# Optimization experiments

Hardware: AMD Instinct MI355X
Metric: run time of the kernel (lower is better)

## Reference

```python
import jax, jax.numpy as jnp
import numpy as np
import math

D_MODEL = 1024
EXPAND = 2
D_INNER = EXPAND * D_MODEL  # 2048
D_STATE = 16
D_CONV = 4
DT_RANK = math.ceil(D_MODEL / 16)  # 64
BATCH = 1
SEQLEN = 2048


def _silu(x):
    return x * jax.nn.sigmoid(x)


def _selective_scan(u, delta, A, B, C, D, z, delta_bias):
    """u, delta, z: (b,d,l); A: (d,n); B, C: (b,n,l); D, delta_bias: (d)."""
    delta = jax.nn.softplus(delta + delta_bias[None, :, None])        # (b,d,l)
    dA = jnp.exp(jnp.einsum('bdl,dn->lbdn', delta, A))                # (l,b,d,n)
    dBu = jnp.einsum('bdl,bnl->lbdn', delta * u, B)                   # (l,b,d,n)
    Ct = jnp.transpose(C, (2, 0, 1))                                  # (l,b,n)

    def step(h, inp):
        dA_t, dBu_t, C_t = inp
        h = dA_t * h + dBu_t                                          # (b,d,n)
        y = jnp.einsum('bdn,bn->bd', h, C_t)
        return h, y

    h0 = jnp.zeros((u.shape[0], u.shape[1], A.shape[1]), dtype=u.dtype)
    _, ys = jax.lax.scan(step, h0, (dA, dBu, Ct))                     # ys: (l,b,d)
    y = jnp.transpose(ys, (1, 2, 0))                                  # (b,d,l)
    y = y + D[:, None] * u
    return y * _silu(z)


def _causal_conv1d(x, conv_w, conv_b):
    """x: (b,d,l); conv_w: (d,w); conv_b: (d). Depthwise causal conv."""
    x_pad = jnp.pad(x, ((0, 0), (0, 0), (D_CONV - 1, 0)))
    kernel = conv_w[:, None, :]  # (d, 1, w)
    y = jax.lax.conv_general_dilated(
        x_pad, kernel, window_strides=(1,), padding='VALID',
        dimension_numbers=('NCH', 'OIH', 'NCH'),
        feature_group_count=D_INNER)
    return y + conv_b[None, :, None]


def setup_inputs() -> dict:
    key = jax.random.key(0)
    ks = jax.random.split(key, 12)
    hidden_states = jax.random.normal(ks[0], (BATCH, SEQLEN, D_MODEL), dtype=jnp.float32)
    in_proj_w = jax.random.normal(ks[1], (2 * D_INNER, D_MODEL), dtype=jnp.float32) * (D_MODEL ** -0.5)
    conv_w = jax.random.normal(ks[2], (D_INNER, D_CONV), dtype=jnp.float32) * (D_CONV ** -0.5)
    conv_b = jnp.zeros((D_INNER,), dtype=jnp.float32)
    dt_std = DT_RANK ** -0.5

    def dt_bias(k):
        dt = jnp.exp(jax.random.uniform(k, (D_INNER,)) * (math.log(0.1) - math.log(0.001)) + math.log(0.001))
        dt = jnp.clip(dt, 1e-4, None)
        return dt + jnp.log(-jnp.expm1(-dt))  # inverse softplus

    A_log = jnp.log(jnp.broadcast_to(jnp.arange(1, D_STATE + 1, dtype=jnp.float32), (D_INNER, D_STATE)))
    x1_proj_w = jax.random.normal(ks[3], (DT_RANK + 2 * D_STATE, D_INNER), dtype=jnp.float32) * (D_INNER ** -0.5)
    dt1_proj_w = jax.random.uniform(ks[4], (D_INNER, DT_RANK), minval=-dt_std, maxval=dt_std)
    dt1_proj_b = dt_bias(ks[5])
    x2_proj_w = jax.random.normal(ks[6], (DT_RANK + 2 * D_STATE, D_INNER), dtype=jnp.float32) * (D_INNER ** -0.5)
    dt2_proj_w = jax.random.uniform(ks[7], (D_INNER, DT_RANK), minval=-dt_std, maxval=dt_std)
    dt2_proj_b = dt_bias(ks[8])
    out_proj_w = jax.random.normal(ks[9], (D_MODEL, D_INNER), dtype=jnp.float32) * (D_INNER ** -0.5)
    return {
        'hidden_states': hidden_states,
        'in_proj_w': in_proj_w, 'conv_w': conv_w, 'conv_b': conv_b,
        'x1_proj_w': x1_proj_w, 'dt1_proj_w': dt1_proj_w, 'dt1_proj_b': dt1_proj_b,
        'A1_log': A_log, 'D1': jnp.ones((D_INNER,), dtype=jnp.float32),
        'x2_proj_w': x2_proj_w, 'dt2_proj_w': dt2_proj_w, 'dt2_proj_b': dt2_proj_b,
        'A2_log': A_log, 'D2': jnp.ones((D_INNER,), dtype=jnp.float32),
        'out_proj_w': out_proj_w,
    }


def reference(hidden_states, in_proj_w, conv_w, conv_b,
              x1_proj_w, dt1_proj_w, dt1_proj_b, A1_log, D1,
              x2_proj_w, dt2_proj_w, dt2_proj_b, A2_log, D2,
              out_proj_w):
    # in_proj: (b,l,d) @ W^T -> (b, 2*d_inner, l)
    xz = jnp.einsum('bld,ed->bel', hidden_states, in_proj_w)
    x, z = jnp.split(xz, 2, axis=1)                                   # (b,d_inner,l) each
    A1 = -jnp.exp(A1_log.astype(jnp.float32))
    A2 = -jnp.exp(A2_log.astype(jnp.float32))
    x = _silu(_causal_conv1d(x, conv_w, conv_b))                      # (b,d_inner,l)

    def branch_params(xp_w, dtp_w):
        dbl = jnp.einsum('bdl,kd->bkl', x, xp_w)                      # (b, r+2n, l)
        dt, Bm, Cm = jnp.split(dbl, [DT_RANK, DT_RANK + D_STATE], axis=1)
        dt = jnp.einsum('brl,dr->bdl', dt, dtp_w)
        return dt, Bm, Cm

    dt1, B1, C1 = branch_params(x1_proj_w, dt1_proj_w)
    dt2, B2, C2 = branch_params(x2_proj_w, dt2_proj_w)
    y1 = _selective_scan(x, dt1, A1, B1, C1, D1.astype(jnp.float32), z, dt1_proj_b.astype(jnp.float32))
    y2 = _selective_scan(x, dt2, A2, B2, C2, D2.astype(jnp.float32), z, dt2_proj_b.astype(jnp.float32))
    y = y1 - y2                                                       # (b,d_inner,l)
    out = jnp.einsum('bdl,od->blo', y, out_proj_w)                    # (b,l,d_model)
    return out
```

## Files before the change

kernel.cpp:

```cpp
#include <hip/hip_runtime.h>
#include <math.h>

#define SEQ 2048
#define DMODEL 1024
#define DIN 2048
#define NST 16
#define DTR 64
#define CH 32
#define NCH (SEQ / CH)
#define LOG2E 1.4426950408889634f

typedef __attribute__((ext_vector_type(8))) _Float16 f16x8;
typedef __attribute__((ext_vector_type(4))) float f32x4;

__device__ __forceinline__ ushort f2h(float f) {
  union { _Float16 h; ushort u; } c; c.h = (_Float16)f; return c.u;
}
__device__ __forceinline__ float h2f(ushort u) {
  union { ushort u; _Float16 h; } c; c.u = u; return (float)c.h;
}
__device__ __forceinline__ float splus(float v) {
  return v > 20.f ? v : log1pf(__expf(v));
}
__device__ __forceinline__ void powers16(float e, float* p) {
  float e2 = e * e, e4 = e2 * e2, e8 = e4 * e4;
  p[0] = e;       p[1] = e2;       p[2] = e2 * e;   p[3] = e4;
  p[4] = e4 * e;  p[5] = e4 * e2;  p[6] = e4 * p[2]; p[7] = e8;
  p[8] = e8 * e;  p[9] = e8 * e2;  p[10] = e8 * p[2]; p[11] = e8 * e4;
  p[12] = e8 * p[4]; p[13] = e8 * p[5]; p[14] = e8 * p[6]; p[15] = e8 * e8;
}

#define GLL(g, l) __builtin_amdgcn_global_load_lds( \
    (const __attribute__((address_space(1))) void*)(g), \
    (__attribute__((address_space(3))) void*)(l), 16, 0, 0)

template<int BM, int BN, int SPLITK, int MODE>
__global__ __launch_bounds__(256, 2) void gemm3p(const ushort* __restrict__ Ahi,
                                                 const ushort* __restrict__ Alo,
                                                 const ushort* __restrict__ Bhi,
                                                 const ushort* __restrict__ Blo,
                                                 float* __restrict__ C,
                                                 int M, int N, int K) {
  constexpr int BK = 32;
  constexpr int WM = BM / 2, WN = BN / 2, TM = WM / 16, TN = WN / 16;
  constexpr int SA = BM / 16, SB = BN / 16;
  constexpr bool dropB = (MODE == 2);
  __shared__ __align__(16) ushort sAh[BM * BK], sAl[BM * BK];
  __shared__ __align__(16) ushort sBh[BN * BK];
  __shared__ __align__(16) ushort sBl[dropB ? 16 : BN * BK];
  const int tid = threadIdx.x, wid = tid >> 6, lane = tid & 63;
  const int m0 = blockIdx.y * BM, n0 = blockIdx.x * BN;
  const int Kc = K / SPLITK, kbeg = blockIdx.z * Kc;
  const int wm0 = (wid >> 1) * WM, wn0 = (wid & 1) * WN;
  const int fr = lane & 15;
  const int lrow = lane >> 2;
  const int lkc = (lane & 3) ^ ((lane >> 3) & 3);
  const int fpo = fr * 32 + (((lane >> 4) ^ ((lane >> 1) & 3)) * 8);

  f32x4 acc[TM][TN], accL[TM][TN];
#pragma unroll
  for (int mi = 0; mi < TM; ++mi)
#pragma unroll
    for (int ni = 0; ni < TN; ++ni)
#pragma unroll
      for (int r = 0; r < 4; ++r) { acc[mi][ni][r] = 0.f; accL[mi][ni][r] = 0.f; }

  for (int k0 = 0; k0 < Kc; k0 += BK) {
    __syncthreads();
    const int kg = kbeg + k0 + lkc * 8;
#pragma unroll
    for (int i = 0; i < SA / 4; ++i) {
      const int seg = wid * (SA / 4) + i;
      const size_t ga = (size_t)(m0 + seg * 16 + lrow) * K + kg;
      GLL(&Ahi[ga], &sAh[seg * 512]);
      GLL(&Alo[ga], &sAl[seg * 512]);
    }
#pragma unroll
    for (int i = 0; i < SB / 4; ++i) {
      const int seg = wid * (SB / 4) + i;
      const size_t ga = (size_t)(n0 + seg * 16 + lrow) * K + kg;
      GLL(&Bhi[ga], &sBh[seg * 512]);
      if constexpr (!dropB) GLL(&Blo[ga], &sBl[seg * 512]);
    }
    __syncthreads();

    f16x8 ah[TM], al[TM], bh[TN], bl[TN];
#pragma unroll
    for (int mi = 0; mi < TM; ++mi) {
      const int r = (wm0 / 16 + mi) * 512 + fpo;
      ah[mi] = *(const f16x8*)&sAh[r];
      al[mi] = *(const f16x8*)&sAl[r];
    }
#pragma unroll
    for (int ni = 0; ni < TN; ++ni) {
      const int r = (wn0 / 16 + ni) * 512 + fpo;
      bh[ni] = *(const f16x8*)&sBh[r];
      if constexpr (!dropB) bl[ni] = *(const f16x8*)&sBl[r];
    }
#pragma unroll
    for (int mi = 0; mi < TM; ++mi)
#pragma unroll
      for (int ni = 0; ni < TN; ++ni) {
        acc[mi][ni] = __builtin_amdgcn_mfma_f32_16x16x32_f16(ah[mi], bh[ni], acc[mi][ni], 0, 0, 0);
        accL[mi][ni] = __builtin_amdgcn_mfma_f32_16x16x32_f16(al[mi], bh[ni], accL[mi][ni], 0, 0, 0);
        if constexpr (!dropB)
          accL[mi][ni] = __builtin_amdgcn_mfma_f32_16x16x32_f16(ah[mi], bl[ni], accL[mi][ni], 0, 0, 0);
      }
  }

  float* __restrict__ Co = C + (size_t)blockIdx.z * M * N;
#pragma unroll
  for (int mi = 0; mi < TM; ++mi)
#pragma unroll
    for (int ni = 0; ni < TN; ++ni)
#pragma unroll
      for (int r = 0; r < 4; ++r)
        Co[(size_t)(m0 + wm0 + mi * 16 + (lane >> 4) * 4 + r) * N + n0 + wn0 + ni * 16 + fr] =
            acc[mi][ni][r] + accL[mi][ni][r] * (1.f / 2048.f);
}

__global__ __launch_bounds__(256, 2) void dt_mfma(const ushort* __restrict__ dtT_hi,
                                                  const ushort* __restrict__ dtT_lo,
                                                  const ushort* __restrict__ dw_hi,
                                                  const ushort* __restrict__ dw_lo,
                                                  const float* __restrict__ b1,
                                                  const float* __restrict__ b2,
                                                  float* __restrict__ o1,
                                                  float* __restrict__ o2) {
  const int br = blockIdx.z;
  const ushort* __restrict__ Ah = dtT_hi + (size_t)br * 131072;
  const ushort* __restrict__ Al_ = dtT_lo + (size_t)br * 131072;
  const ushort* __restrict__ Bh = dw_hi + (size_t)br * 131072;
  const ushort* __restrict__ Bl = dw_lo + (size_t)br * 131072;
  const float* __restrict__ bias = br ? b2 : b1;
  float* __restrict__ o = br ? o2 : o1;
  __shared__ __align__(16) ushort sAh[128 * 32], sAl[128 * 32];
  __shared__ __align__(16) ushort sBh[128 * 32], sBl[128 * 32];
  const int tid = threadIdx.x, wid = tid >> 6, lane = tid & 63;
  const int m0 = blockIdx.y * 128, n0 = blockIdx.x * 128;
  const int wm0 = (wid >> 1) * 64, wn0 = (wid & 1) * 64;
  const int fr = lane & 15;
  const int lrow = lane >> 2;
  const int lkc = (lane & 3) ^ ((lane >> 3) & 3);
  const int fpo = fr * 32 + (((lane >> 4) ^ ((lane >> 1) & 3)) * 8);

  f32x4 acc[4][4], accL[4][4];
#pragma unroll
  for (int mi = 0; mi < 4; ++mi)
#pragma unroll
    for (int ni = 0; ni < 4; ++ni)
#pragma unroll
      for (int r = 0; r < 4; ++r) { acc[mi][ni][r] = 0.f; accL[mi][ni][r] = 0.f; }

  for (int k0 = 0; k0 < 64; k0 += 32) {
    __syncthreads();
    const int kg = k0 + lkc * 8;
#pragma unroll
    for (int i = 0; i < 2; ++i) {
      const int seg = wid * 2 + i;
      const size_t ga = (size_t)(m0 + seg * 16 + lrow) * 64 + kg;
      GLL(&Ah[ga], &sAh[seg * 512]);
      GLL(&Al_[ga], &sAl[seg * 512]);
      const size_t gb = (size_t)(n0 + seg * 16 + lrow) * 64 + kg;
      GLL(&Bh[gb], &sBh[seg * 512]);
      GLL(&Bl[gb], &sBl[seg * 512]);
    }
    __syncthreads();

    f16x8 ah[4], al[4], bh[4], bl[4];
#pragma unroll
    for (int mi = 0; mi < 4; ++mi) {
      const int r = (wm0 / 16 + mi) * 512 + fpo;
      ah[mi] = *(const f16x8*)&sAh[r];
      al[mi] = *(const f16x8*)&sAl[r];
    }
#pragma unroll
    for (int ni = 0; ni < 4; ++ni) {
      const int r = (wn0 / 16 + ni) * 512 + fpo;
      bh[ni] = *(const f16x8*)&sBh[r];
      bl[ni] = *(const f16x8*)&sBl[r];
    }
#pragma unroll
    for (int mi = 0; mi < 4; ++mi)
#pragma unroll
      for (int ni = 0; ni < 4; ++ni) {
        acc[mi][ni] = __builtin_amdgcn_mfma_f32_16x16x32_f16(ah[mi], bh[ni], acc[mi][ni], 0, 0, 0);
        accL[mi][ni] = __builtin_amdgcn_mfma_f32_16x16x32_f16(al[mi], bh[ni], accL[mi][ni], 0, 0, 0);
        accL[mi][ni] = __builtin_amdgcn_mfma_f32_16x16x32_f16(ah[mi], bl[ni], accL[mi][ni], 0, 0, 0);
      }
  }

#pragma unroll
  for (int ni = 0; ni < 4; ++ni) {
    const int n = n0 + wn0 + ni * 16 + fr;
    const float bv = bias[n];
#pragma unroll
    for (int mi = 0; mi < 4; ++mi)
#pragma unroll
      for (int r = 0; r < 4; ++r) {
        const int m = m0 + wm0 + mi * 16 + (lane >> 4) * 4 + r;
        o[(size_t)m * DIN + n] = splus(acc[mi][ni][r] + accL[mi][ni][r] * (1.f / 2048.f) + bv);
      }
  }
}

__device__ __forceinline__ void split_store4h(float4 v, ushort* hi, ushort* lo, size_t i) {
  ushort h0 = f2h(v.x), h1 = f2h(v.y), h2 = f2h(v.z), h3 = f2h(v.w);
  *(ushort4*)&hi[i] = make_ushort4(h0, h1, h2, h3);
  *(ushort4*)&lo[i] = make_ushort4(f2h((v.x - h2f(h0)) * 2048.f), f2h((v.y - h2f(h1)) * 2048.f),
                                   f2h((v.z - h2f(h2)) * 2048.f), f2h((v.w - h2f(h3)) * 2048.f));
}

__global__ __launch_bounds__(256) void cvt_fused(const float* __restrict__ inw,
                                                 const float* __restrict__ hid,
                                                 const float* __restrict__ x1w,
                                                 const float* __restrict__ x2w,
                                                 const float* __restrict__ dtw1,
                                                 const float* __restrict__ dtw2,
                                                 ushort* __restrict__ w_hi, ushort* __restrict__ w_lo,
                                                 ushort* __restrict__ h_hi,
                                                 ushort* __restrict__ wx_hi, ushort* __restrict__ wx_lo,
                                                 ushort* __restrict__ dw_hi, ushort* __restrict__ dw_lo) {
  const int q = blockIdx.x * 256 + threadIdx.x;
  if (q >= 1048576 && q < 1572864) {
    const size_t i = (size_t)(q - 1048576) * 4;
    float4 v = *(const float4*)&hid[i];
    *(ushort4*)&h_hi[i] = make_ushort4(f2h(v.x), f2h(v.y), f2h(v.z), f2h(v.w));
    return;
  }
  const float* src; ushort* dhi; ushort* dlo; int base;
  if (q < 1048576)       { src = inw; dhi = w_hi;  dlo = w_lo;  base = q; }
  else if (q < 1622016)  { src = x1w; dhi = wx_hi; dlo = wx_lo; base = q - 1572864; }
  else if (q < 1671168)  { src = x2w; dhi = wx_hi + 196608; dlo = wx_lo + 196608; base = q - 1622016; }
  else if (q < 1703936)  { src = dtw1; dhi = dw_hi; dlo = dw_lo; base = q - 1671168; }
  else                   { src = dtw2; dhi = dw_hi + 131072; dlo = dw_lo + 131072; base = q - 1703936; }
  const size_t i = (size_t)base * 4;
  split_store4h(*(const float4*)&src[i], dhi, dlo, i);
}

__global__ __launch_bounds__(256) void reduce_out(const float* __restrict__ p,
                                                  float* __restrict__ o, int n) {
  const int i = (blockIdx.x * 256 + threadIdx.x) * 4;
  if (i >= n) return;
  float4 a = *(const float4*)&p[i];
  float4 b = *(const float4*)&p[(size_t)n + i];
  float4 c = *(const float4*)&p[(size_t)2 * n + i];
  float4 d = *(const float4*)&p[(size_t)3 * n + i];
  *(float4*)&o[i] = make_float4(a.x + b.x + c.x + d.x, a.y + b.y + c.y + d.y,
                                a.z + b.z + c.z + d.z, a.w + b.w + c.w + d.w);
}

__global__ __launch_bounds__(256) void conv_tr_kernel(const float* __restrict__ xz,
                                                      const float* __restrict__ cw,
                                                      const float* __restrict__ cb,
                                                      ushort* __restrict__ xcT_hi,
                                                      ushort* __restrict__ xcT_lo,
                                                      float* __restrict__ zsT) {
  const int l0 = blockIdx.x * 64, d0 = blockIdx.y * 64;
  const int tid = threadIdx.x;
  __shared__ float xin[64][68];
  __shared__ float To[64][65];
  __shared__ float cwS[64][4];
  __shared__ float cbS[64];

  for (int i = tid; i < 1024; i += 256) {
    const int d = i >> 4, q = i & 15;
    float4 v = *(const float4*)&xz[(size_t)(d0 + d) * SEQ + l0 + q * 4];
    xin[d][3 + q * 4 + 0] = v.x; xin[d][3 + q * 4 + 1] = v.y;
    xin[d][3 + q * 4 + 2] = v.z; xin[d][3 + q * 4 + 3] = v.w;
  }
  if (tid < 192) {
    const int j = tid >> 6, d = tid & 63;
    const int l = l0 - 3 + j;
    xin[d][j] = (l >= 0) ? xz[(size_t)(d0 + d) * SEQ + l] : 0.f;
  }
  if (tid < 64) {
    cbS[tid] = cb[d0 + tid];
    float4 w = *(const float4*)&cw[(d0 + tid) * 4];
    cwS[tid][0] = w.x; cwS[tid][1] = w.y; cwS[tid][2] = w.z; cwS[tid][3] = w.w;
  }
  __syncthreads();

  for (int i = tid; i < 4096; i += 256) {
    const int d = i >> 6, l = i & 63;
    float a = cbS[d] + cwS[d][0] * xin[d][l] + cwS[d][1] * xin[d][l + 1] +
              cwS[d][2] * xin[d][l + 2] + cwS[d][3] * xin[d][l + 3];
    To[d][l] = a / (1.f + __expf(-a));
  }
  __syncthreads();

  for (int i = tid; i < 4096; i += 256) {
    const int l = i >> 6, dd = i & 63;
    float v = To[dd][l];
    ushort h = f2h(v);
    xcT_hi[(size_t)(l0 + l) * DIN + d0 + dd] = h;
    xcT_lo[(size_t)(l0 + l) * DIN + d0 + dd] = f2h((v - h2f(h)) * 2048.f);
  }
  __syncthreads();

  for (int i = tid; i < 1024; i += 256) {
    const int d = i >> 4, q = i & 15;
    float4 v = *(const float4*)&xz[(size_t)(DIN + d0 + d) * SEQ + l0 + q * 4];
    To[d][q * 4 + 0] = v.x / (1.f + __expf(-v.x));
    To[d][q * 4 + 1] = v.y / (1.f + __expf(-v.y));
    To[d][q * 4 + 2] = v.z / (1.f + __expf(-v.z));
    To[d][q * 4 + 3] = v.w / (1.f + __expf(-v.w));
  }
  __syncthreads();
  for (int i = tid; i < 4096; i += 256) {
    const int l = i >> 6, dd = i & 63;
    zsT[(size_t)(l0 + l) * DIN + d0 + dd] = To[dd][l];
  }
}

__global__ __launch_bounds__(256) void reduce_dblT_kernel(const float* __restrict__ p,
                                                          float* __restrict__ BT1,
                                                          float* __restrict__ CT1,
                                                          float* __restrict__ BT2,
                                                          float* __restrict__ CT2,
                                                          ushort* __restrict__ dtT_hi,
                                                          ushort* __restrict__ dtT_lo) {
  const int NE = SEQ * 192;
  const int idx = blockIdx.x * 256 + threadIdx.x;
  float s = 0.f;
#pragma unroll
  for (int cc = 0; cc < 8; ++cc) s += p[(size_t)cc * NE + idx];
  const int l = idx / 192, k = idx - l * 192;
  if (k < 64) {
    const size_t off = (size_t)l * 64 + k;
    const ushort hh = f2h(s);
    dtT_hi[off] = hh; dtT_lo[off] = f2h((s - h2f(hh)) * 2048.f);
  } else if (k < 80)  BT1[l * NST + (k - 64)] = s;
  else if (k < 96)    CT1[l * NST + (k - 80)] = s;
  else if (k < 160) {
    const size_t off = 131072 + (size_t)l * 64 + (k - 96);
    const ushort hh = f2h(s);
    dtT_hi[off] = hh; dtT_lo[off] = f2h((s - h2f(hh)) * 2048.f);
  }
  else if (k < 176)   BT2[l * NST + (k - 160)] = s;
  else                CT2[l * NST + (k - 176)] = s;
}

__global__ __launch_bounds__(256) void scan_phase_a(const ushort* __restrict__ uhi,
                                                    const ushort* __restrict__ ulo,
                                                    const float* __restrict__ sp1T,
                                                    const float* __restrict__ sp2T,
                                                    const float* __restrict__ BT1,
                                                    const float* __restrict__ BT2,
                                                    const float* __restrict__ Al1,
                                                    const float* __restrict__ Al2,
                                                    float* __restrict__ hend,
                                                    float* __restrict__ Pend) {
  const int c = blockIdx.y, t0 = c * CH;
  const int d = blockIdx.x * 256 + threadIdx.x;
  const size_t gbase = (size_t)t0 * DIN + d;

  __shared__ __align__(16) float Bs[2][CH][NST];
  {
    const int j = threadIdx.x;
    if (j < 128) ((float4*)&Bs[0][0][0])[j] = ((const float4*)&BT1[(size_t)t0 * NST])[j];
    else ((float4*)&Bs[1][0][0])[j - 128] = ((const float4*)&BT2[(size_t)t0 * NST])[j - 128];
  }
  __syncthreads();

  bool fast = true;
#pragma unroll
  for (int n = 0; n < NST; ++n) {
    float k1 = __expf(Al1[(size_t)d * NST + n]);
    float k2 = __expf(Al2[(size_t)d * NST + n]);
    fast = fast && (fabsf(k1 - (float)(n + 1)) < 1e-3f) && (fabsf(k2 - (float)(n + 1)) < 1e-3f);
  }
  float h1[NST], h2[NST];
#pragma unroll
  for (int n = 0; n < NST; ++n) { h1[n] = 0.f; h2[n] = 0.f; }
  float S1 = 0.f, S2 = 0.f;

  if (fast) {
    for (int tt = 0; tt < CH / 4; ++tt) {
      float s1[4], s2[4], ua[4];
#pragma unroll
      for (int j = 0; j < 4; ++j) {
        const size_t idx = gbase + (size_t)(tt * 4 + j) * DIN;
        s1[j] = sp1T[idx]; s2[j] = sp2T[idx];
        ua[j] = h2f(uhi[idx]) + h2f(ulo[idx]) * (1.f / 2048.f);
      }
#pragma unroll
      for (int j = 0; j < 4; ++j) {
        const int t = tt * 4 + j;
        S1 += s1[j]; S2 += s2[j];
        const float spu1 = s1[j] * ua[j], spu2 = s2[j] * ua[j];
        float p[NST];
        powers16(__expf(-s1[j]), p);
#pragma unroll
        for (int n = 0; n < NST; ++n) h1[n] = fmaf(p[n], h1[n], spu1 * Bs[0][t][n]);
        powers16(__expf(-s2[j]), p);
#pragma unroll
        for (int n = 0; n < NST; ++n) h2[n] = fmaf(p[n], h2[n], spu2 * Bs[1][t][n]);
      }
    }
  } else {
    float A1e[NST], A2e[NST];
#pragma unroll
    for (int n = 0; n < NST; ++n) {
      A1e[n] = -__expf(Al1[(size_t)d * NST + n]) * LOG2E;
      A2e[n] = -__expf(Al2[(size_t)d * NST + n]) * LOG2E;
    }
    for (int tt = 0; tt < CH / 4; ++tt) {
      float s1[4], s2[4], ua[4];
#pragma unroll
      for (int j = 0; j < 4; ++j) {
        const size_t idx = gbase + (size_t)(tt * 4 + j) * DIN;
        s1[j] = sp1T[idx]; s2[j] = sp2T[idx];
        ua[j] = h2f(uhi[idx]) + h2f(ulo[idx]) * (1.f / 2048.f);
      }
#pragma unroll
      for (int j = 0; j < 4; ++j) {
        const int t = tt * 4 + j;
        S1 += s1[j]; S2 += s2[j];
        const float spu1 = s1[j] * ua[j], spu2 = s2[j] * ua[j];
#pragma unroll
        for (int n = 0; n < NST; ++n) {
          h1[n] = fmaf(exp2f(A1e[n] * s1[j]), h1[n], spu1 * Bs[0][t][n]);
          h2[n] = fmaf(exp2f(A2e[n] * s2[j]), h2[n], spu2 * Bs[1][t][n]);
        }
      }
    }
  }

  float P1[NST], P2[NST];
  if (fast) {
    powers16(__expf(-S1), P1);
    powers16(__expf(-S2), P2);
  } else {
#pragma unroll
    for (int n = 0; n < NST; ++n) {
      P1[n] = exp2f(-__expf(Al1[(size_t)d * NST + n]) * LOG2E * S1);
      P2[n] = exp2f(-__expf(Al2[(size_t)d * NST + n]) * LOG2E * S2);
    }
  }
  const size_t b1 = ((size_t)c * DIN + d) * NST;
  const size_t b2 = ((size_t)(NCH + c) * DIN + d) * NST;
#pragma unroll
  for (int n = 0; n < NST; n += 4) {
    *(float4*)&hend[b1 + n] = make_float4(h1[n], h1[n + 1], h1[n + 2], h1[n + 3]);
    *(float4*)&Pend[b1 + n] = make_float4(P1[n], P1[n + 1], P1[n + 2], P1[n + 3]);
    *(float4*)&hend[b2 + n] = make_float4(h2[n], h2[n + 1], h2[n + 2], h2[n + 3]);
    *(float4*)&Pend[b2 + n] = make_float4(P2[n], P2[n + 1], P2[n + 2], P2[n + 3]);
  }
}

__global__ __launch_bounds__(256) void carry_cvt(const float* __restrict__ hend,
                                                 float* __restrict__ PendHin,
                                                 const float* __restrict__ outw,
                                                 ushort* __restrict__ ow_hi) {
  const int b = blockIdx.x;
  if (b < 256) {
    const int flat = b * 256 + threadIdx.x;
    const int br = flat >> 15;
    const int dn = flat & 32767;
    float h = 0.f;
    for (int c = 0; c < NCH; ++c) {
      size_t idx = ((size_t)(br * NCH + c) << 15) + dn;
      float Pv = PendHin[idx];
      float he = hend[idx];
      PendHin[idx] = h;
      h = fmaf(Pv, h, he);
    }
  } else {
    const size_t i = ((size_t)(b - 256) * 256 + threadIdx.x) * 4;
    float4 v = *(const float4*)&outw[i];
    *(ushort4*)&ow_hi[i] = make_ushort4(f2h(v.x), f2h(v.y), f2h(v.z), f2h(v.w));
  }
}

__global__ __launch_bounds__(256) void scan_phase_c(const ushort* __restrict__ uhi,
                                                    const ushort* __restrict__ ulo,
                                                    const float* __restrict__ sp1T,
                                                    const float* __restrict__ sp2T,
                                                    const float* __restrict__ BT1,
                                                    const float* __restrict__ CT1,
                                                    const float* __restrict__ BT2,
                                                    const float* __restrict__ CT2,
                                                    const float* __restrict__ Al1,
                                                    const float* __restrict__ Al2,
                                                    const float* __restrict__ D1,
                                                    const float* __restrict__ D2,
                                                    const float* __restrict__ hin,
                                                    const float* __restrict__ zsT,
                                                    ushort* __restrict__ yd_hi,
                                                    ushort* __restrict__ yd_lo) {
  const int c = blockIdx.y, t0 = c * CH;
  const int d = blockIdx.x * 256 + threadIdx.x;
  const size_t gbase = (size_t)t0 * DIN + d;

  __shared__ __align__(16) float Bs[2][CH][NST];
  __shared__ __align__(16) float Cs[2][CH][NST];
  {
    const int j = threadIdx.x;
    if (j < 128) {
      ((float4*)&Bs[0][0][0])[j] = ((const float4*)&BT1[(size_t)t0 * NST])[j];
      ((float4*)&Cs[0][0][0])[j] = ((const float4*)&CT1[(size_t)t0 * NST])[j];
    } else {
      ((float4*)&Bs[1][0][0])[j - 128] = ((const float4*)&BT2[(size_t)t0 * NST])[j - 128];
      ((float4*)&Cs[1][0][0])[j - 128] = ((const float4*)&CT2[(size_t)t0 * NST])[j - 128];
    }
  }
  __syncthreads();

  bool fast = true;
#pragma unroll
  for (int n = 0; n < NST; ++n) {
    float k1 = __expf(Al1[(size_t)d * NST + n]);
    float k2 = __expf(Al2[(size_t)d * NST + n]);
    fast = fast && (fabsf(k1 - (float)(n + 1)) < 1e-3f) && (fabsf(k2 - (float)(n + 1)) < 1e-3f);
  }
  const float Ddd = D1[d] - D2[d];
  float h1[NST], h2[NST];
  const size_t hb1 = ((size_t)c * DIN + d) * NST;
  const size_t hb2 = ((size_t)(NCH + c) * DIN + d) * NST;
#pragma unroll
  for (int n = 0; n < NST; n += 4) {
    float4 v1 = *(const float4*)&hin[hb1 + n];
    h1[n] = v1.x; h1[n + 1] = v1.y; h1[n + 2] = v1.z; h1[n + 3] = v1.w;
    float4 v2 = *(const float4*)&hin[hb2 + n];
    h2[n] = v2.x; h2[n + 1] = v2.y; h2[n + 2] = v2.z; h2[n + 3] = v2.w;
  }

  if (fast) {
    for (int tt = 0; tt < CH / 4; ++tt) {
      float s1[4], s2[4], ua[4];
#pragma unroll
      for (int j = 0; j < 4; ++j) {
        const size_t idx = gbase + (size_t)(tt * 4 + j) * DIN;
        s1[j] = sp1T[idx]; s2[j] = sp2T[idx];
        ua[j] = h2f(uhi[idx]) + h2f(ulo[idx]) * (1.f / 2048.f);
      }
#pragma unroll
      for (int j = 0; j < 4; ++j) {
        const int t = tt * 4 + j;
        const size_t idx = gbase + (size_t)t * DIN;
        const float spu1 = s1[j] * ua[j], spu2 = s2[j] * ua[j];
        float p[NST];
        float y1 = 0.f, y2 = 0.f;
        powers16(__expf(-s1[j]), p);
#pragma unroll
        for (int n = 0; n < NST; ++n) {
          h1[n] = fmaf(p[n], h1[n], spu1 * Bs[0][t][n]);
          y1 = fmaf(h1[n], Cs[0][t][n], y1);
        }
        powers16(__expf(-s2[j]), p);
#pragma unroll
        for (int n = 0; n < NST; ++n) {
          h2[n] = fmaf(p[n], h2[n], spu2 * Bs[1][t][n]);
          y2 = fmaf(h2[n], Cs[1][t][n], y2);
        }
        const float yd = (y1 - y2 + Ddd * ua[j]) * zsT[idx];
        const ushort hh = f2h(yd);
        yd_hi[idx] = hh;
        yd_lo[idx] = f2h((yd - h2f(hh)) * 2048.f);
      }
    }
  } else {
    float A1e[NST], A2e[NST];
#pragma unroll
    for (int n = 0; n < NST; ++n) {
      A1e[n] = -__expf(Al1[(size_t)d * NST + n]) * LOG2E;
      A2e[n] = -__expf(Al2[(size_t)d * NST + n]) * LOG2E;
    }
    for (int tt = 0; tt < CH / 4; ++tt) {
      float s1[4], s2[4], ua[4];
#pragma unroll
      for (int j = 0; j < 4; ++j) {
        const size_t idx = gbase + (size_t)(tt * 4 + j) * DIN;
        s1[j] = sp1T[idx]; s2[j] = sp2T[idx];
        ua[j] = h2f(uhi[idx]) + h2f(ulo[idx]) * (1.f / 2048.f);
      }
#pragma unroll
      for (int j = 0; j < 4; ++j) {
        const int t = tt * 4 + j;
        const size_t idx = gbase + (size_t)t * DIN;
        const float spu1 = s1[j] * ua[j], spu2 = s2[j] * ua[j];
        float y1 = 0.f, y2 = 0.f;
#pragma unroll
        for (int n = 0; n < NST; ++n) {
          h1[n] = fmaf(exp2f(A1e[n] * s1[j]), h1[n], spu1 * Bs[0][t][n]);
          y1 = fmaf(h1[n], Cs[0][t][n], y1);
          h2[n] = fmaf(exp2f(A2e[n] * s2[j]), h2[n], spu2 * Bs[1][t][n]);
          y2 = fmaf(h2[n], Cs[1][t][n], y2);
        }
        const float yd = (y1 - y2 + Ddd * ua[j]) * zsT[idx];
        const ushort hh = f2h(yd);
        yd_hi[idx] = hh;
        yd_lo[idx] = f2h((yd - h2f(hh)) * 2048.f);
      }
    }
  }
}

extern "C" void kernel_launch(void* const* d_in, const int* in_sizes, int n_in,
                              void* d_out, int out_size, void* d_ws, size_t ws_size,
                              hipStream_t stream) {
  const float* hidden = (const float*)d_in[0];
  const float* in_proj_w = (const float*)d_in[1];
  const float* conv_w = (const float*)d_in[2];
  const float* conv_b = (const float*)d_in[3];
  const float* x1w = (const float*)d_in[4];
  const float* dtw1 = (const float*)d_in[5];
  const float* dtb1 = (const float*)d_in[6];
  const float* Al1 = (const float*)d_in[7];
  const float* D1 = (const float*)d_in[8];
  const float* x2w = (const float*)d_in[9];
  const float* dtw2 = (const float*)d_in[10];
  const float* dtb2 = (const float*)d_in[11];
  const float* Al2 = (const float*)d_in[12];
  const float* D2 = (const float*)d_in[13];
  const float* outw = (const float*)d_in[14];
  float* out = (float*)d_out;

  float* ws = (float*)d_ws;
  float* xz = ws;
  float* xcTbuf = xz + (size_t)4096 * SEQ;
  float* dtTbuf = xcTbuf + (size_t)SEQ * DIN;
  float* sp1T = dtTbuf + (size_t)192 * SEQ;
  float* sp2T = sp1T + (size_t)SEQ * DIN;
  float* siluzT = sp2T + (size_t)SEQ * DIN;
  float* hendB = siluzT + (size_t)SEQ * DIN;
  float* PendB = hendB + (size_t)2 * NCH * DIN * NST;
  float* BT1 = PendB + (size_t)2 * NCH * DIN * NST;
  float* CT1 = BT1 + (size_t)SEQ * NST;
  float* BT2 = CT1 + (size_t)SEQ * NST;
  float* CT2 = BT2 + (size_t)SEQ * NST;
  float* wxp = CT2 + (size_t)SEQ * NST;

  ushort* xcT_hi = (ushort*)xcTbuf;
  ushort* xcT_lo = (ushort*)(xcTbuf + 2097152);
  ushort* dtT_hi = (ushort*)dtTbuf;
  ushort* dtT_lo = dtT_hi + 262144;
  ushort* w_hi = (ushort*)siluzT;
  ushort* w_lo = (ushort*)(siluzT + 2097152);
  ushort* h_hi = (ushort*)hendB;
  ushort* dw_hi = ((ushort*)hendB) + 2097152;
  ushort* dw_lo = dw_hi + 262144;
  ushort* wx_hi = (ushort*)wxp;
  ushort* wx_lo = (ushort*)(wxp + 196608);
  float* xp_part = sp1T;
  ushort* yd_hi = (ushort*)xcTbuf;
  ushort* yd_lo = (ushort*)(xcTbuf + 2097152);
  ushort* ow_hi = (ushort*)xz;
  float* opart = sp1T;

  dim3 blk(256);

  cvt_fused<<<dim3(6784), blk, 0, stream>>>(in_proj_w, hidden, x1w, x2w, dtw1, dtw2,
                                            w_hi, w_lo, h_hi, wx_hi, wx_lo, dw_hi, dw_lo);

  gemm3p<128, 128, 1, 2><<<dim3(SEQ / 128, 4096 / 128, 1), blk, 0, stream>>>(
      w_hi, w_lo, h_hi, h_hi, xz, 4096, SEQ, DMODEL);

  conv_tr_kernel<<<dim3(SEQ / 64, DIN / 64), blk, 0, stream>>>(
      xz, conv_w, conv_b, xcT_hi, xcT_lo, siluzT);

  gemm3p<128, 64, 8, 0><<<dim3(192 / 64, SEQ / 128, 8), blk, 0, stream>>>(
      xcT_hi, xcT_lo, wx_hi, wx_lo, xp_part, SEQ, 192, DIN);

  reduce_dblT_kernel<<<dim3(192 * SEQ / 256), blk, 0, stream>>>(
      xp_part, BT1, CT1, BT2, CT2, dtT_hi, dtT_lo);

  dt_mfma<<<dim3(DIN / 128, SEQ / 128, 2), blk, 0, stream>>>(
      dtT_hi, dtT_lo, dw_hi, dw_lo, dtb1, dtb2, sp1T, sp2T);

  scan_phase_a<<<dim3(DIN / 256, NCH), blk, 0, stream>>>(
      xcT_hi, xcT_lo, sp1T, sp2T, BT1, BT2, Al1, Al2, hendB, PendB);
  carry_cvt<<<dim3(2304), blk, 0, stream>>>(hendB, PendB, outw, ow_hi);
  scan_phase_c<<<dim3(DIN / 256, NCH), blk, 0, stream>>>(
      xcT_hi, xcT_lo, sp1T, sp2T, BT1, CT1, BT2, CT2, Al1, Al2, D1, D2,
      PendB, siluzT, yd_hi, yd_lo);

  gemm3p<128, 128, 4, 2><<<dim3(DMODEL / 128, SEQ / 128, 4), blk, 0, stream>>>(
      yd_hi, yd_lo, ow_hi, ow_hi, opart, SEQ, DMODEL, DIN);
  reduce_out<<<dim3(SEQ * DMODEL / 1024), blk, 0, stream>>>(opart, out, SEQ * DMODEL);
}
```

Measured before the change: 331.7 us.

## Store softplus(dt) and silu(z) as fp16 hi/lo pairs; add XCD block swizzle

The softplus(dt) outputs for both branches and the silu(z) intermediate are now written as two fp16 halves (high plus scaled residual) instead of fp32, and the scan kernels rebuild them on load. Total bytes stay the same, but each read becomes two 2-byte loads from separate arrays, which adds instructions and conversions. Separately, the GEMM and dt kernels remap block indices so that neighbouring tiles land on the same XCD, aiming for better L2 reuse. The buffer aliasing in the launcher was updated to fit the new split arrays.

```diff
diff --git a/kernel.cpp b/kernel.cpp
--- a/kernel.cpp
+++ b/kernel.cpp
@@ -33,6 +33,13 @@
 #define GLL(g, l) __builtin_amdgcn_global_load_lds( \
     (const __attribute__((address_space(1))) void*)(g), \
     (__attribute__((address_space(3))) void*)(l), 16, 0, 0)
+
+#define XCD_SWZ(BMv, BNv)                                              \
+  const int nwg_ = gridDim.x * gridDim.y;                              \
+  const int flat_ = blockIdx.y * gridDim.x + blockIdx.x;               \
+  const int swz_ = (flat_ & 7) * (nwg_ >> 3) + (flat_ >> 3);           \
+  const int m0 = (swz_ / gridDim.x) * (BMv);                           \
+  const int n0 = (swz_ % gridDim.x) * (BNv);
 
 template<int BM, int BN, int SPLITK, int MODE>
 __global__ __launch_bounds__(256, 2) void gemm3p(const ushort* __restrict__ Ahi,
@@ -49,7 +56,7 @@
   __shared__ __align__(16) ushort sBh[BN * BK];
   __shared__ __align__(16) ushort sBl[dropB ? 16 : BN * BK];
   const int tid = threadIdx.x, wid = tid >> 6, lane = tid & 63;
-  const int m0 = blockIdx.y * BM, n0 = blockIdx.x * BN;
+  XCD_SWZ(BM, BN)
   const int Kc = K / SPLITK, kbeg = blockIdx.z * Kc;
   const int wm0 = (wid >> 1) * WM, wn0 = (wid & 1) * WN;
   const int fr = lane & 15;
@@ -125,19 +132,22 @@
                                                   const ushort* __restrict__ dw_lo,
                                                   const float* __restrict__ b1,
                                                   const float* __restrict__ b2,
-                                                  float* __restrict__ o1,
-                                                  float* __restrict__ o2) {
+                                                  ushort* __restrict__ sp1h,
+                                                  ushort* __restrict__ sp1l,
+                                                  ushort* __restrict__ sp2h,
+                                                  ushort* __restrict__ sp2l) {
   const int br = blockIdx.z;
   const ushort* __restrict__ Ah = dtT_hi + (size_t)br * 131072;
   const ushort* __restrict__ Al_ = dtT_lo + (size_t)br * 131072;
   const ushort* __restrict__ Bh = dw_hi + (size_t)br * 131072;
   const ushort* __restrict__ Bl = dw_lo + (size_t)br * 131072;
   const float* __restrict__ bias = br ? b2 : b1;
-  float* __restrict__ o = br ? o2 : o1;
+  ushort* __restrict__ ohi = br ? sp2h : sp1h;
+  ushort* __restrict__ olo = br ? sp2l : sp1l;
   __shared__ __align__(16) ushort sAh[128 * 32], sAl[128 * 32];
   __shared__ __align__(16) ushort sBh[128 * 32], sBl[128 * 32];
   const int tid = threadIdx.x, wid = tid >> 6, lane = tid & 63;
-  const int m0 = blockIdx.y * 128, n0 = blockIdx.x * 128;
+  XCD_SWZ(128, 128)
   const int wm0 = (wid >> 1) * 64, wn0 = (wid & 1) * 64;
   const int fr = lane & 15;
   const int lrow = lane >> 2;
@@ -199,7 +209,11 @@
 #pragma unroll
       for (int r = 0; r < 4; ++r) {
         const int m = m0 + wm0 + mi * 16 + (lane >> 4) * 4 + r;
-        o[(size_t)m * DIN + n] = splus(acc[mi][ni][r] + accL[mi][ni][r] * (1.f / 2048.f) + bv);
+        const float v = splus(acc[mi][ni][r] + accL[mi][ni][r] * (1.f / 2048.f) + bv);
+        const ushort hh = f2h(v);
+        const size_t o = (size_t)m * DIN + n;
+        ohi[o] = hh;
+        olo[o] = f2h((v - h2f(hh)) * 2048.f);
       }
   }
 }
@@ -255,7 +269,8 @@
                                                       const float* __restrict__ cb,
                                                       ushort* __restrict__ xcT_hi,
                                                       ushort* __restrict__ xcT_lo,
-                                                      float* __restrict__ zsT) {
+                                                      ushort* __restrict__ zs_hi,
+                                                      ushort* __restrict__ zs_lo) {
   const int l0 = blockIdx.x * 64, d0 = blockIdx.y * 64;
   const int tid = threadIdx.x;
   __shared__ float xin[64][68];
@@ -309,7 +324,11 @@
   __syncthreads();
   for (int i = tid; i < 4096; i += 256) {
     const int l = i >> 6, dd = i & 63;
-    zsT[(size_t)(l0 + l) * DIN + d0 + dd] = To[dd][l];
+    float v = To[dd][l];
+    const size_t o = (size_t)(l0 + l) * DIN + d0 + dd;
+    ushort h = f2h(v);
+    zs_hi[o] = h;
+    zs_lo[o] = f2h((v - h2f(h)) * 2048.f);
   }
 }
 
@@ -343,8 +362,10 @@
 
 __global__ __launch_bounds__(256) void scan_phase_a(const ushort* __restrict__ uhi,
                                                     const ushort* __restrict__ ulo,
-                                                    const float* __restrict__ sp1T,
-                                                    const float* __restrict__ sp2T,
+                                                    const ushort* __restrict__ sp1h,
+                                                    const ushort* __restrict__ sp1l,
+                                                    const ushort* __restrict__ sp2h,
+                                                    const ushort* __restrict__ sp2l,
                                                     const float* __restrict__ BT1,
                                                     const float* __restrict__ BT2,
                                                     const float* __restrict__ Al1,
@@ -381,7 +402,8 @@
 #pragma unroll
       for (int j = 0; j < 4; ++j) {
         const size_t idx = gbase + (size_t)(tt * 4 + j) * DIN;
-        s1[j] = sp1T[idx]; s2[j] = sp2T[idx];
+        s1[j] = h2f(sp1h[idx]) + h2f(sp1l[idx]) * (1.f / 2048.f);
+        s2[j] = h2f(sp2h[idx]) + h2f(sp2l[idx]) * (1.f / 2048.f);
         ua[j] = h2f(uhi[idx]) + h2f(ulo[idx]) * (1.f / 2048.f);
       }
 #pragma unroll
@@ -410,7 +432,8 @@
 #pragma unroll
       for (int j = 0; j < 4; ++j) {
         const size_t idx = gbase + (size_t)(tt * 4 + j) * DIN;
-        s1[j] = sp1T[idx]; s2[j] = sp2T[idx];
+        s1[j] = h2f(sp1h[idx]) + h2f(sp1l[idx]) * (1.f / 2048.f);
+        s2[j] = h2f(sp2h[idx]) + h2f(sp2l[idx]) * (1.f / 2048.f);
         ua[j] = h2f(uhi[idx]) + h2f(ulo[idx]) * (1.f / 2048.f);
       }
 #pragma unroll
@@ -475,8 +498,10 @@
 
 __global__ __launch_bounds__(256) void scan_phase_c(const ushort* __restrict__ uhi,
                                                     const ushort* __restrict__ ulo,
-                                                    const float* __restrict__ sp1T,
-                                                    const float* __restrict__ sp2T,
+                                                    const ushort* __restrict__ sp1h,
+                                                    const ushort* __restrict__ sp1l,
+                                                    const ushort* __restrict__ sp2h,
+                                                    const ushort* __restrict__ sp2l,
                                                     const float* __restrict__ BT1,
                                                     const float* __restrict__ CT1,
                                                     const float* __restrict__ BT2,
@@ -486,7 +511,8 @@
                                                     const float* __restrict__ D1,
                                                     const float* __restrict__ D2,
                                                     const float* __restrict__ hin,
-                                                    const float* __restrict__ zsT,
+                                                    const ushort* __restrict__ zsh,
+                                                    const ushort* __restrict__ zsl,
                                                     ushort* __restrict__ yd_hi,
                                                     ushort* __restrict__ yd_lo) {
   const int c = blockIdx.y, t0 = c * CH;
@@ -532,7 +558,8 @@
 #pragma unroll
       for (int j = 0; j < 4; ++j) {
         const size_t idx = gbase + (size_t)(tt * 4 + j) * DIN;
-        s1[j] = sp1T[idx]; s2[j] = sp2T[idx];
+        s1[j] = h2f(sp1h[idx]) + h2f(sp1l[idx]) * (1.f / 2048.f);
+        s2[j] = h2f(sp2h[idx]) + h2f(sp2l[idx]) * (1.f / 2048.f);
         ua[j] = h2f(uhi[idx]) + h2f(ulo[idx]) * (1.f / 2048.f);
       }
 #pragma unroll
@@ -554,7 +581,8 @@
           h2[n] = fmaf(p[n], h2[n], spu2 * Bs[1][t][n]);
           y2 = fmaf(h2[n], Cs[1][t][n], y2);
         }
-        const float yd = (y1 - y2 + Ddd * ua[j]) * zsT[idx];
+        const float zv = h2f(zsh[idx]) + h2f(zsl[idx]) * (1.f / 2048.f);
+        const float yd = (y1 - y2 + Ddd * ua[j]) * zv;
         const ushort hh = f2h(yd);
         yd_hi[idx] = hh;
         yd_lo[idx] = f2h((yd - h2f(hh)) * 2048.f);
@@ -572,7 +600,8 @@
 #pragma unroll
       for (int j = 0; j < 4; ++j) {
         const size_t idx = gbase + (size_t)(tt * 4 + j) * DIN;
-        s1[j] = sp1T[idx]; s2[j] = sp2T[idx];
+        s1[j] = h2f(sp1h[idx]) + h2f(sp1l[idx]) * (1.f / 2048.f);
+        s2[j] = h2f(sp2h[idx]) + h2f(sp2l[idx]) * (1.f / 2048.f);
         ua[j] = h2f(uhi[idx]) + h2f(ulo[idx]) * (1.f / 2048.f);
       }
 #pragma unroll
@@ -588,7 +617,8 @@
           h2[n] = fmaf(exp2f(A2e[n] * s2[j]), h2[n], spu2 * Bs[1][t][n]);
           y2 = fmaf(h2[n], Cs[1][t][n], y2);
         }
-        const float yd = (y1 - y2 + Ddd * ua[j]) * zsT[idx];
+        const float zv = h2f(zsh[idx]) + h2f(zsl[idx]) * (1.f / 2048.f);
+        const float yd = (y1 - y2 + Ddd * ua[j]) * zv;
         const ushort hh = f2h(yd);
         yd_hi[idx] = hh;
         yd_lo[idx] = f2h((yd - h2f(hh)) * 2048.f);
@@ -621,10 +651,10 @@
   float* xz = ws;
   float* xcTbuf = xz + (size_t)4096 * SEQ;
   float* dtTbuf = xcTbuf + (size_t)SEQ * DIN;
-  float* sp1T = dtTbuf + (size_t)192 * SEQ;
-  float* sp2T = sp1T + (size_t)SEQ * DIN;
-  float* siluzT = sp2T + (size_t)SEQ * DIN;
-  float* hendB = siluzT + (size_t)SEQ * DIN;
+  float* spbuf1 = dtTbuf + (size_t)192 * SEQ;
+  float* spbuf2 = spbuf1 + (size_t)SEQ * DIN;
+  float* zsbuf = spbuf2 + (size_t)SEQ * DIN;
+  float* hendB = zsbuf + (size_t)SEQ * DIN;
   float* PendB = hendB + (size_t)2 * NCH * DIN * NST;
   float* BT1 = PendB + (size_t)2 * NCH * DIN * NST;
   float* CT1 = BT1 + (size_t)SEQ * NST;
@@ -636,19 +666,24 @@
   ushort* xcT_lo = (ushort*)(xcTbuf + 2097152);
   ushort* dtT_hi = (ushort*)dtTbuf;
   ushort* dtT_lo = dtT_hi + 262144;
-  ushort* w_hi = (ushort*)siluzT;
-  ushort* w_lo = (ushort*)(siluzT + 2097152);
+  ushort* sp1h = (ushort*)spbuf1;
+  ushort* sp1l = sp1h + (size_t)SEQ * DIN;
+  ushort* sp2h = (ushort*)spbuf2;
+  ushort* sp2l = sp2h + (size_t)SEQ * DIN;
+  ushort* zs_hi = (ushort*)zsbuf;
+  ushort* zs_lo = zs_hi + (size_t)SEQ * DIN;
+  ushort* w_hi = (ushort*)zsbuf;
+  ushort* w_lo = (ushort*)(zsbuf + 2097152);
   ushort* h_hi = (ushort*)hendB;
   ushort* dw_hi = ((ushort*)hendB) + 2097152;
   ushort* dw_lo = dw_hi + 262144;
   ushort* wx_hi = (ushort*)wxp;
   ushort* wx_lo = (ushort*)(wxp + 196608);
-  float* xp_part = sp1T;
+  float* xp_part = spbuf1;
   ushort* yd_hi = (ushort*)xcTbuf;
   ushort* yd_lo = (ushort*)(xcTbuf + 2097152);
   ushort* ow_hi = (ushort*)xz;
-  float* opart = sp1T;
-
+  float* opart = spbuf1;
   dim3 blk(256);
 
   cvt_fused<<<dim3(6784), blk, 0, stream>>>(in_proj_w, hidden, x1w, x2w, dtw1, dtw2,
@@ -658,7 +693,7 @@
       w_hi, w_lo, h_hi, h_hi, xz, 4096, SEQ, DMODEL);
 
   conv_tr_kernel<<<dim3(SEQ / 64, DIN / 64), blk, 0, stream>>>(
-      xz, conv_w, conv_b, xcT_hi, xcT_lo, siluzT);
+      xz, conv_w, conv_b, xcT_hi, xcT_lo, zs_hi, zs_lo);
 
   gemm3p<128, 64, 8, 0><<<dim3(192 / 64, SEQ / 128, 8), blk, 0, stream>>>(
       xcT_hi, xcT_lo, wx_hi, wx_lo, xp_part, SEQ, 192, DIN);
@@ -667,14 +702,14 @@
       xp_part, BT1, CT1, BT2, CT2, dtT_hi, dtT_lo);
 
   dt_mfma<<<dim3(DIN / 128, SEQ / 128, 2), blk, 0, stream>>>(
-      dtT_hi, dtT_lo, dw_hi, dw_lo, dtb1, dtb2, sp1T, sp2T);
+      dtT_hi, dtT_lo, dw_hi, dw_lo, dtb1, dtb2, sp1h, sp1l, sp2h, sp2l);
 
   scan_phase_a<<<dim3(DIN / 256, NCH), blk, 0, stream>>>(
-      xcT_hi, xcT_lo, sp1T, sp2T, BT1, BT2, Al1, Al2, hendB, PendB);
+      xcT_hi, xcT_lo, sp1h, sp1l, sp2h, sp2l, BT1, BT2, Al1, Al2, hendB, PendB);
   carry_cvt<<<dim3(2304), blk, 0, stream>>>(hendB, PendB, outw, ow_hi);
   scan_phase_c<<<dim3(DIN / 256, NCH), blk, 0, stream>>>(
-      xcT_hi, xcT_lo, sp1T, sp2T, BT1, CT1, BT2, CT2, Al1, Al2, D1, D2,
-      PendB, siluzT, yd_hi, yd_lo);
+      xcT_hi, xcT_lo, sp1h, sp1l, sp2h, sp2l, BT1, CT1, BT2, CT2, Al1, Al2,
+      D1, D2, PendB, zs_hi, zs_lo, yd_hi, yd_lo);
 
   gemm3p<128, 128, 4, 2><<<dim3(DMODEL / 128, SEQ / 128, 4), blk, 0, stream>>>(
       yd_hi, yd_lo, ow_hi, ow_hi, opart, SEQ, DMODEL, DIN);
```

New measurement: 341.9 us. +3.1%, slower.
